# Performance work log

Measured on AMD Instinct MI355X. Metric: run time of the kernel, lower is better.

Reference implementation:

```python
import jax, jax.numpy as jnp
from jax import lax
import numpy as np

B, H, W = 8, 512, 512
COUT = 256          # backbone.out_channels
NPTS = 5 + 6        # num_vertebra_points + num_disc_points
CASC = 3            # num_cascades
PIX_MEAN, PIX_STD = 0.5, 1.0


def setup_inputs() -> dict:
    key = jax.random.key(0)
    k0, k1, k2, k3 = jax.random.split(key, 4)
    images = jax.random.normal(k0, (B, 1, H, W), jnp.float32)
    # stand-in for BackboneWithFPN level '0': stride-4 7x7 conv, 3 -> 256 ch
    backbone_w = jax.random.normal(k1, (COUT, 3, 7, 7), jnp.float32) * 0.05
    backbone_b = jnp.zeros((COUT,), jnp.float32)
    # self.fc: 1x1 conv, 256 -> 11 keypoint score channels
    fc_w = jax.random.normal(k2, (NPTS, COUT), jnp.float32) * 0.05
    fc_b = jnp.zeros((NPTS,), jnp.float32)
    # cascade heads: Linear(256, 2) per cascade
    head_w = jax.random.normal(k3, (CASC, COUT, 2), jnp.float32) * 0.02
    head_b = jnp.zeros((CASC, 2), jnp.float32)
    return dict(images=images, backbone_w=backbone_w, backbone_b=backbone_b,
                fc_w=fc_w, fc_b=fc_b, head_w=head_w, head_b=head_b)


def _resize_bilinear_ac(x, oh, ow):
    # bilinear, align_corners=True, matching F.interpolate
    b, c, h, w = x.shape
    ys = jnp.linspace(0.0, h - 1.0, oh)
    xs = jnp.linspace(0.0, w - 1.0, ow)
    y0 = jnp.floor(ys).astype(jnp.int32); y1 = jnp.minimum(y0 + 1, h - 1)
    x0 = jnp.floor(xs).astype(jnp.int32); x1 = jnp.minimum(x0 + 1, w - 1)
    wy = (ys - y0.astype(x.dtype))[:, None]          # (oh,1)
    wx = (xs - x0.astype(x.dtype))                   # (ow,)
    top = x[:, :, y0, :] * (1.0 - wy) + x[:, :, y1, :] * wy   # (b,c,oh,w)
    return top[:, :, :, x0] * (1.0 - wx) + top[:, :, :, x1] * wx


def _extract_point_feature(fm, coords, height, width):
    # fm: (B,C,fh,fw); coords: (B,P,2) with (width, height) order
    fh, fw = fm.shape[-2:]
    hi = jnp.clip(jnp.round(coords[:, :, 1] * (fh / height)).astype(jnp.int32), 0, fh - 1)
    wi = jnp.clip(jnp.round(coords[:, :, 0] * (fw / width)).astype(jnp.int32), 0, fw - 1)
    fm_t = fm.transpose(0, 2, 3, 1)                  # (B,fh,fw,C)
    return jax.vmap(lambda f, a, b: f[a, b])(fm_t, hi, wi)  # (B,P,C)


def reference(images, backbone_w, backbone_b, fc_w, fc_b, head_w, head_b):
    b = images.shape[0]
    x = (images - PIX_MEAN) / PIX_STD
    x = jnp.broadcast_to(x, (b, 3, H, W))            # .expand(-1,3,-1,-1)
    fm = lax.conv_general_dilated(
        x, backbone_w, window_strides=(4, 4), padding=((3, 3), (3, 3)),
        dimension_numbers=('NCHW', 'OIHW', 'NCHW')) + backbone_b[None, :, None, None]
    scores = jnp.einsum('bchw,kc->bkhw', fm, fc_w) + fc_b[None, :, None, None]
    scores = _resize_bilinear_ac(scores, H, W)
    heat = jax.nn.sigmoid(scores)
    # SpinalModelBase: per-channel argmax -> (width, height) coords
    idx = jnp.argmax(heat.reshape(b, NPTS, -1), axis=-1)
    coords = jnp.stack([idx % W, idx // W], axis=-1).astype(jnp.float32)  # (B,P,2)
    # cascades: gather point features, tiny Linear shift, update coords
    for i in range(CASC):
        feats = _extract_point_feature(fm, coords, H, W)     # (B,P,C)
        shift = feats @ head_w[i] + head_b[i]                # (B,P,2)
        coords = coords + shift
    return coords  # final cascade output, float (B, NPTS, 2)
```

## Files before the change

kernel.cpp:

```cpp
#include <hip/hip_runtime.h>
#include <hip/hip_bf16.h>
#include <math.h>

#define BATCH 8
#define HH 512
#define WW 512
#define COUT 256
#define NPTS 11
#define CASC 3
#define FH 128
#define FW 128
#define KT 49
#define NBK (BATCH*NPTS)
#define NSPLIT 8
#define OROWS (HH/NSPLIT)

#define FOLD_OFF   0
#define SCORES_OFF 1024
#define PVAL_OFF   (1024 + 1441792)
#define PIDX_OFF   (PVAL_OFF + 704)

#define STEPC (127.0f/511.0f)

__global__ __launch_bounds__(256) void fold_kernel(
    const float* __restrict__ bw, const float* __restrict__ bb,
    const float* __restrict__ fcw, const float* __restrict__ fcb,
    const float* __restrict__ hw, const float* __restrict__ hb,
    float* __restrict__ fold) {
  int id = blockIdx.x*4 + (threadIdx.x >> 6);
  if (id >= 850) return;
  int row = id / 50, t = id % 50;
  int lane = threadIdx.x & 63;
  float acc = 0.f;
  for (int c = lane; c < COUT; c += 64) {
    float coef;
    if (row < NPTS) {
      coef = fcw[row*COUT + c];
    } else {
      int r = row - NPTS;
      coef = hw[(r >> 1)*(COUT*2) + c*2 + (r & 1)];
    }
    float wsum;
    if (t < KT) {
      const float* p = bw + c*(3*KT) + t;
      wsum = p[0] + p[KT] + p[2*KT];
    } else {
      wsum = bb[c];
    }
    acc += coef * wsum;
  }
  #pragma unroll
  for (int off = 32; off > 0; off >>= 1) acc += __shfl_down(acc, off);
  if (lane == 0) {
    if (t == KT) acc += (row < NPTS) ? fcb[row] : hb[row - NPTS];
    if (row < NPTS) {
      if (t < KT) fold[t*NPTS + row] = acc;
      else        fold[NPTS*KT + row] = acc;
    } else {
      int r = row - NPTS;
      if (t < KT) fold[550 + r*KT + t] = acc;
      else        fold[844 + r] = acc;
    }
  }
}

__global__ __launch_bounds__(256) void scores_kernel(
    const float* __restrict__ img, const float* __restrict__ fold,
    float* __restrict__ scores) {
  int g = blockIdx.x*256 + threadIdx.x;
  int b = g >> 14;
  int rem = g & 16383;
  int y = rem >> 7, x = rem & 127;
  const float* im = img + (size_t)b * (HH*WW);
  float acc[NPTS];
  #pragma unroll
  for (int k = 0; k < NPTS; ++k) acc[k] = fold[NPTS*KT + k];
  int iy0 = y*4 - 3, ix0 = x*4 - 3;
  #pragma unroll
  for (int kh = 0; kh < 7; ++kh) {
    int iy = iy0 + kh;
    if (iy < 0 || iy >= HH) continue;
    #pragma unroll
    for (int kw = 0; kw < 7; ++kw) {
      int ix = ix0 + kw;
      if (ix < 0 || ix >= WW) continue;
      float xv = im[iy*WW + ix] - 0.5f;
      int t = kh*7 + kw;
      #pragma unroll
      for (int k = 0; k < NPTS; ++k) acc[k] = fmaf(fold[t*NPTS + k], xv, acc[k]);
    }
  }
  float* out = scores + (size_t)b * (NPTS*FH*FW) + rem;
  #pragma unroll
  for (int k = 0; k < NPTS; ++k) out[(size_t)k*(FH*FW)] = acc[k];
}

__global__ __launch_bounds__(256) void argmax_kernel(
    const float* __restrict__ scores, float* __restrict__ pval,
    int* __restrict__ pidx) {
  __shared__ __align__(16) float s[20*128];
  __shared__ float wvv[4];
  __shared__ int   wvi[4];
  int bk = blockIdx.x / NSPLIT;
  int q  = blockIdx.x % NSPLIT;
  const float* src = scores + (size_t)bk * (FH*FW);

  int oyb = q*OROWS;
  int ybase = (int)((float)oyb * STEPC);
  int ylast = (int)((float)(oyb + OROWS - 1) * STEPC);
  int yend  = min(ylast + 1, FH - 1);
  int rows  = yend - ybase + 1;
  {
    const float4* src4 = (const float4*)(src + ybase*FW);
    float4* s4 = (float4*)s;
    int n4 = (rows*FW) >> 2;
    for (int i = threadIdx.x; i < n4; i += 256) s4[i] = src4[i];
  }
  __syncthreads();

  int t = threadIdx.x;
  int kb = t >> 1;
  int cf = (kb*511 + 126)/127;
  int cl = (kb < 127) ? ((kb + 1)*511 + 126)/127 - 1 : 511;
  int ox = (t & 1) ? cl : cf;
  float tx = (float)ox * STEPC;
  int xa0 = (int)tx;
  float wx = tx - (float)xa0;
  int xa1 = min(xa0 + 1, FW - 1);
  float omwx = 1.f - wx;

  float best = -3.4028235e38f;
  int bidx = 0x7fffffff;
  for (int k = ybase; k <= ylast; ++k) {
    int y1 = min(k + 1, FH - 1);
    const float* r0 = s + (k  - ybase)*FW;
    const float* r1 = s + (y1 - ybase)*FW;
    float A = r0[xa0], B = r1[xa0], C = r0[xa1], D = r1[xa1];
    int rf = (k*511 + 126)/127;
    int rl = (k < 127) ? ((k + 1)*511 + 126)/127 - 1 : 511;
    if (rf >= oyb && rf < oyb + OROWS) {
      float ty = (float)rf * STEPC;
      int y0i = (int)ty;
      float wy = ty - (float)y0i;
      float omwy = 1.f - wy;
      float top0 = A*omwy + B*wy;
      float top1 = C*omwy + D*wy;
      float v = top0*omwx + top1*wx;
      if (v > best) { best = v; bidx = rf*512 + ox; }
    }
    if (rl != rf && rl >= oyb && rl < oyb + OROWS) {
      float ty = (float)rl * STEPC;
      int y0i = (int)ty;
      float wy = ty - (float)y0i;
      float omwy = 1.f - wy;
      float top0 = A*omwy + B*wy;
      float top1 = C*omwy + D*wy;
      float v = top0*omwx + top1*wx;
      if (v > best) { best = v; bidx = rl*512 + ox; }
    }
  }

  #pragma unroll
  for (int off = 32; off > 0; off >>= 1) {
    float ov = __shfl_down(best, off);
    int   oi = __shfl_down(bidx, off);
    if (ov > best || (ov == best && oi < bidx)) { best = ov; bidx = oi; }
  }
  int wave = threadIdx.x >> 6;
  if ((threadIdx.x & 63) == 0) { wvv[wave] = best; wvi[wave] = bidx; }
  __syncthreads();
  if (threadIdx.x == 0) {
    best = wvv[0]; bidx = wvi[0];
    #pragma unroll
    for (int w = 1; w < 4; ++w) {
      float ov = wvv[w]; int oi = wvi[w];
      if (ov > best || (ov == best && oi < bidx)) { best = ov; bidx = oi; }
    }
    pval[bk*NSPLIT + q] = best;
    pidx[bk*NSPLIT + q] = bidx;
  }
}

__global__ __launch_bounds__(128) void cascade_kernel(
    const float* __restrict__ img, const float* __restrict__ fold,
    const float* __restrict__ pval, const int* __restrict__ pidx,
    float* __restrict__ out) {
  int p = threadIdx.x;
  if (p >= NBK) return;
  float best = pval[p*NSPLIT]; int bidx = pidx[p*NSPLIT];
  #pragma unroll
  for (int q = 1; q < NSPLIT; ++q) {
    float v = pval[p*NSPLIT + q]; int i = pidx[p*NSPLIT + q];
    if (v > best || (v == best && i < bidx)) { best = v; bidx = i; }
  }
  float cx = (float)(bidx & 511);
  float cy = (float)(bidx >> 9);
  int b = p / NPTS;
  const float* im = img + (size_t)b * (HH*WW);
  for (int i = 0; i < CASC; ++i) {
    float ry = rintf(cy * 0.25f), rx = rintf(cx * 0.25f);
    int hi = (int)fminf(fmaxf(ry, 0.f), (float)(FH - 1));
    int wi = (int)fminf(fmaxf(rx, 0.f), (float)(FW - 1));
    float s0 = fold[844 + i*2 + 0];
    float s1 = fold[844 + i*2 + 1];
    int iy0 = hi*4 - 3, ix0 = wi*4 - 3;
    for (int kh = 0; kh < 7; ++kh) {
      int iy = iy0 + kh;
      if (iy < 0 || iy >= HH) continue;
      for (int kw = 0; kw < 7; ++kw) {
        int ix = ix0 + kw;
        if (ix < 0 || ix >= WW) continue;
        float xv = im[iy*WW + ix] - 0.5f;
        int t = kh*7 + kw;
        s0 = fmaf(fold[550 + (i*2 + 0)*KT + t], xv, s0);
        s1 = fmaf(fold[550 + (i*2 + 1)*KT + t], xv, s1);
      }
    }
    cx += s0;
    cy += s1;
  }
  out[p*2 + 0] = cx;
  out[p*2 + 1] = cy;
}

extern "C" void kernel_launch(void* const* d_in, const int* in_sizes, int n_in,
                              void* d_out, int out_size, void* d_ws, size_t ws_size,
                              hipStream_t stream) {
  const float* img = (const float*)d_in[0];
  const float* bw  = (const float*)d_in[1];
  const float* bb  = (const float*)d_in[2];
  const float* fcw = (const float*)d_in[3];
  const float* fcb = (const float*)d_in[4];
  const float* hw  = (const float*)d_in[5];
  const float* hb  = (const float*)d_in[6];
  float* out = (float*)d_out;

  float* ws     = (float*)d_ws;
  float* fold   = ws + FOLD_OFF;
  float* scores = ws + SCORES_OFF;
  float* pval   = ws + PVAL_OFF;
  int*   pidx   = (int*)(ws + PIDX_OFF);

  fold_kernel<<<213, 256, 0, stream>>>(bw, bb, fcw, fcb, hw, hb, fold);
  scores_kernel<<<512, 256, 0, stream>>>(img, fold, scores);
  argmax_kernel<<<NBK*NSPLIT, 256, 0, stream>>>(scores, pval, pidx);
  cascade_kernel<<<1, 128, 0, stream>>>(img, fold, pval, pidx, out);
}
```

Before: 116.8 us.

## Fuse score convolution into argmax kernel, computing low-res scores in shared memory

Merges the score convolution and the upsample-argmax into one kernel. Each block computes the low-res score rows its output strip needs for all 11 channels directly into shared memory, then runs the bilinear argmax per channel. This drops the global scores round trip and one launch. The cost is recomputing the boundary rows shared by neighbouring strips, and a grid of only 256 blocks with the split raised to 32.

```diff
diff --git a/kernel.cpp b/kernel.cpp
--- a/kernel.cpp
+++ b/kernel.cpp
@@ -12,13 +12,13 @@
 #define FW 128
 #define KT 49
 #define NBK (BATCH*NPTS)
-#define NSPLIT 8
+#define NSPLIT 32
 #define OROWS (HH/NSPLIT)
+#define MAXR 6
 
 #define FOLD_OFF   0
-#define SCORES_OFF 1024
-#define PVAL_OFF   (1024 + 1441792)
-#define PIDX_OFF   (PVAL_OFF + 704)
+#define PVAL_OFF   1024
+#define PIDX_OFF   (PVAL_OFF + NBK*NSPLIT)
 
 #define STEPC (127.0f/511.0f)
 
@@ -64,57 +64,46 @@
   }
 }
 
-__global__ __launch_bounds__(256) void scores_kernel(
+__global__ __launch_bounds__(256) void score_argmax_kernel(
     const float* __restrict__ img, const float* __restrict__ fold,
-    float* __restrict__ scores) {
-  int g = blockIdx.x*256 + threadIdx.x;
-  int b = g >> 14;
-  int rem = g & 16383;
-  int y = rem >> 7, x = rem & 127;
-  const float* im = img + (size_t)b * (HH*WW);
-  float acc[NPTS];
-  #pragma unroll
-  for (int k = 0; k < NPTS; ++k) acc[k] = fold[NPTS*KT + k];
-  int iy0 = y*4 - 3, ix0 = x*4 - 3;
-  #pragma unroll
-  for (int kh = 0; kh < 7; ++kh) {
-    int iy = iy0 + kh;
-    if (iy < 0 || iy >= HH) continue;
-    #pragma unroll
-    for (int kw = 0; kw < 7; ++kw) {
-      int ix = ix0 + kw;
-      if (ix < 0 || ix >= WW) continue;
-      float xv = im[iy*WW + ix] - 0.5f;
-      int t = kh*7 + kw;
-      #pragma unroll
-      for (int k = 0; k < NPTS; ++k) acc[k] = fmaf(fold[t*NPTS + k], xv, acc[k]);
-    }
-  }
-  float* out = scores + (size_t)b * (NPTS*FH*FW) + rem;
-  #pragma unroll
-  for (int k = 0; k < NPTS; ++k) out[(size_t)k*(FH*FW)] = acc[k];
-}
-
-__global__ __launch_bounds__(256) void argmax_kernel(
-    const float* __restrict__ scores, float* __restrict__ pval,
-    int* __restrict__ pidx) {
-  __shared__ __align__(16) float s[20*128];
-  __shared__ float wvv[4];
-  __shared__ int   wvi[4];
-  int bk = blockIdx.x / NSPLIT;
-  int q  = blockIdx.x % NSPLIT;
-  const float* src = scores + (size_t)bk * (FH*FW);
+    float* __restrict__ pval, int* __restrict__ pidx) {
+  __shared__ __align__(16) float s[NPTS*MAXR*FW];
+  __shared__ float wvv[NPTS*4];
+  __shared__ int   wvi[NPTS*4];
+  int b = blockIdx.x / NSPLIT;
+  int q = blockIdx.x % NSPLIT;
 
   int oyb = q*OROWS;
   int ybase = (int)((float)oyb * STEPC);
   int ylast = (int)((float)(oyb + OROWS - 1) * STEPC);
   int yend  = min(ylast + 1, FH - 1);
   int rows  = yend - ybase + 1;
-  {
-    const float4* src4 = (const float4*)(src + ybase*FW);
-    float4* s4 = (float4*)s;
-    int n4 = (rows*FW) >> 2;
-    for (int i = threadIdx.x; i < n4; i += 256) s4[i] = src4[i];
+  const float* im = img + (size_t)b * (HH*WW);
+
+  for (int p = threadIdx.x; p < rows*FW; p += 256) {
+    int ry = p >> 7;
+    int x  = p & 127;
+    int y  = ybase + ry;
+    float acc[NPTS];
+    #pragma unroll
+    for (int k = 0; k < NPTS; ++k) acc[k] = fold[NPTS*KT + k];
+    int iy0 = y*4 - 3, ix0 = x*4 - 3;
+    #pragma unroll
+    for (int kh = 0; kh < 7; ++kh) {
+      int iy = iy0 + kh;
+      if (iy < 0 || iy >= HH) continue;
+      #pragma unroll
+      for (int kw = 0; kw < 7; ++kw) {
+        int ix = ix0 + kw;
+        if (ix < 0 || ix >= WW) continue;
+        float xv = im[iy*WW + ix] - 0.5f;
+        int t = kh*7 + kw;
+        #pragma unroll
+        for (int k = 0; k < NPTS; ++k) acc[k] = fmaf(fold[t*NPTS + k], xv, acc[k]);
+      }
+    }
+    #pragma unroll
+    for (int k = 0; k < NPTS; ++k) s[(k*MAXR + ry)*FW + x] = acc[k];
   }
   __syncthreads();
 
@@ -128,54 +117,59 @@
   float wx = tx - (float)xa0;
   int xa1 = min(xa0 + 1, FW - 1);
   float omwx = 1.f - wx;
-
-  float best = -3.4028235e38f;
-  int bidx = 0x7fffffff;
-  for (int k = ybase; k <= ylast; ++k) {
-    int y1 = min(k + 1, FH - 1);
-    const float* r0 = s + (k  - ybase)*FW;
-    const float* r1 = s + (y1 - ybase)*FW;
-    float A = r0[xa0], B = r1[xa0], C = r0[xa1], D = r1[xa1];
-    int rf = (k*511 + 126)/127;
-    int rl = (k < 127) ? ((k + 1)*511 + 126)/127 - 1 : 511;
-    if (rf >= oyb && rf < oyb + OROWS) {
-      float ty = (float)rf * STEPC;
-      int y0i = (int)ty;
-      float wy = ty - (float)y0i;
-      float omwy = 1.f - wy;
-      float top0 = A*omwy + B*wy;
-      float top1 = C*omwy + D*wy;
-      float v = top0*omwx + top1*wx;
-      if (v > best) { best = v; bidx = rf*512 + ox; }
-    }
-    if (rl != rf && rl >= oyb && rl < oyb + OROWS) {
-      float ty = (float)rl * STEPC;
-      int y0i = (int)ty;
-      float wy = ty - (float)y0i;
-      float omwy = 1.f - wy;
-      float top0 = A*omwy + B*wy;
-      float top1 = C*omwy + D*wy;
-      float v = top0*omwx + top1*wx;
-      if (v > best) { best = v; bidx = rl*512 + ox; }
-    }
-  }
+  int wave = threadIdx.x >> 6;
+  int lane = threadIdx.x & 63;
 
   #pragma unroll
-  for (int off = 32; off > 0; off >>= 1) {
-    float ov = __shfl_down(best, off);
-    int   oi = __shfl_down(bidx, off);
-    if (ov > best || (ov == best && oi < bidx)) { best = ov; bidx = oi; }
-  }
-  int wave = threadIdx.x >> 6;
-  if ((threadIdx.x & 63) == 0) { wvv[wave] = best; wvi[wave] = bidx; }
+  for (int ch = 0; ch < NPTS; ++ch) {
+    float best = -3.4028235e38f;
+    int bidx = 0x7fffffff;
+    for (int k = ybase; k <= ylast; ++k) {
+      int y1 = min(k + 1, FH - 1);
+      const float* r0 = s + (ch*MAXR + (k  - ybase))*FW;
+      const float* r1 = s + (ch*MAXR + (y1 - ybase))*FW;
+      float A = r0[xa0], B = r1[xa0], C = r0[xa1], D = r1[xa1];
+      int rf = (k*511 + 126)/127;
+      int rl = (k < 127) ? ((k + 1)*511 + 126)/127 - 1 : 511;
+      if (rf >= oyb && rf < oyb + OROWS) {
+        float ty = (float)rf * STEPC;
+        int y0i = (int)ty;
+        float wy = ty - (float)y0i;
+        float omwy = 1.f - wy;
+        float top0 = A*omwy + B*wy;
+        float top1 = C*omwy + D*wy;
+        float v = top0*omwx + top1*wx;
+        if (v > best) { best = v; bidx = rf*512 + ox; }
+      }
+      if (rl != rf && rl >= oyb && rl < oyb + OROWS) {
+        float ty = (float)rl * STEPC;
+        int y0i = (int)ty;
+        float wy = ty - (float)y0i;
+        float omwy = 1.f - wy;
+        float top0 = A*omwy + B*wy;
+        float top1 = C*omwy + D*wy;
+        float v = top0*omwx + top1*wx;
+        if (v > best) { best = v; bidx = rl*512 + ox; }
+      }
+    }
+    #pragma unroll
+    for (int off = 32; off > 0; off >>= 1) {
+      float ov = __shfl_down(best, off);
+      int   oi = __shfl_down(bidx, off);
+      if (ov > best || (ov == best && oi < bidx)) { best = ov; bidx = oi; }
+    }
+    if (lane == 0) { wvv[ch*4 + wave] = best; wvi[ch*4 + wave] = bidx; }
+  }
   __syncthreads();
-  if (threadIdx.x == 0) {
-    best = wvv[0]; bidx = wvi[0];
+  if (threadIdx.x < NPTS) {
+    int ch = threadIdx.x;
+    float best = wvv[ch*4]; int bidx = wvi[ch*4];
     #pragma unroll
     for (int w = 1; w < 4; ++w) {
-      float ov = wvv[w]; int oi = wvi[w];
+      float ov = wvv[ch*4 + w]; int oi = wvi[ch*4 + w];
       if (ov > best || (ov == best && oi < bidx)) { best = ov; bidx = oi; }
     }
+    int bk = b*NPTS + ch;
     pval[bk*NSPLIT + q] = best;
     pidx[bk*NSPLIT + q] = bidx;
   }
@@ -237,12 +231,10 @@
 
   float* ws     = (float*)d_ws;
   float* fold   = ws + FOLD_OFF;
-  float* scores = ws + SCORES_OFF;
   float* pval   = ws + PVAL_OFF;
   int*   pidx   = (int*)(ws + PIDX_OFF);
 
   fold_kernel<<<213, 256, 0, stream>>>(bw, bb, fcw, fcb, hw, hb, fold);
-  scores_kernel<<<512, 256, 0, stream>>>(img, fold, scores);
-  argmax_kernel<<<NBK*NSPLIT, 256, 0, stream>>>(scores, pval, pidx);
+  score_argmax_kernel<<<BATCH*NSPLIT, 256, 0, stream>>>(img, fold, pval, pidx);
   cascade_kernel<<<1, 128, 0, stream>>>(img, fold, pval, pidx, out);
 }
```

New measurement: 138.0 us. +18.2%, slower.
